# Performance work log

Hardware: AMD Instinct MI355X
Metric: run time of the kernel (lower is better)

Reference implementation:

```python
import jax, jax.numpy as jnp
import numpy as np

EPS = 1e-12  # guard sqrt at zero distance


def setup_inputs() -> dict:
    key = jax.random.key(0)
    k1, k2 = jax.random.split(key)
    B, C, N = 4, 3, 8192
    predict_pc = jax.random.normal(k1, (B, C, N), dtype=jnp.float32)
    gt_pc = jax.random.normal(k2, (B, C, N), dtype=jnp.float32)
    return {"predict_pc": predict_pc, "gt_pc": gt_pc}


def reference(predict_pc, gt_pc):
    # predict_pc: [B, 3, Np], gt_pc: [B, 3, Ng]
    B = gt_pc.shape[0]
    Np = predict_pc.shape[2]
    Ng = gt_pc.shape[2]
    denom = B * (Ng + Np)

    # Pairwise Euclidean distances d[b, n, m] = ||predict[b,:,n] - gt[b,:,m]||
    # via the |p|^2 + |g|^2 - 2 p.g expansion (avoids [B,3,Np,Ng] intermediate).
    p2 = jnp.sum(predict_pc * predict_pc, axis=1)            # [B, Np]
    g2 = jnp.sum(gt_pc * gt_pc, axis=1)                      # [B, Ng]
    dot = jnp.einsum('bcn,bcm->bnm', predict_pc, gt_pc)      # [B, Np, Ng]
    d2 = p2[:, :, None] + g2[:, None, :] - 2.0 * dot         # [B, Np, Ng]
    d = jnp.sqrt(jnp.maximum(d2, EPS))

    # z: for each gt point, distance to nearest predicted point -> min over Np
    z = jnp.min(d, axis=1)   # [B, Ng]
    # z_2: for each predicted point, distance to nearest gt point -> min over Ng
    z2 = jnp.min(d, axis=2)  # [B, Np]

    loss = z.sum() / denom + z2.sum() / denom
    return loss
```

## Files before the change

kernel.cpp:

```cpp
#include <hip/hip_runtime.h>
#include <math.h>


#define B_        4
#define N_        8192
#define THREADS   256
#define ROWS_PB   256
#define ROWBLKS   (N_ / ROWS_PB)
#define MRANGE    1024
#define MSPLIT    (N_ / MRANGE)
#define MTILES    (MRANGE / 16)
#define NGROUPS   B_
#define BLKS_PER_GROUP (ROWBLKS * MSPLIT)
#define POISON    0xAAAAAAAAu
#define INF_BITS  0x7F800000u

typedef __bf16 bf16x8 __attribute__((ext_vector_type(8)));
typedef float  f32x4  __attribute__((ext_vector_type(4)));

#define SM_ZERO   0
#define SM_A      16
#define SM_B      8208
#define SM_COL    40976
#define SM_ROW    45072
#define SM_BYTES  46096

__device__ __forceinline__ unsigned short bf16_rne(float f) {
    unsigned u = __float_as_uint(f);
    return (unsigned short)((u + 0x7FFFu + ((u >> 16) & 1u)) >> 16);
}
__device__ __forceinline__ float bf16_tof(unsigned short h) {
    return __uint_as_float(((unsigned)h) << 16);
}

__device__ __forceinline__ void slotsA(const float* base, int n, unsigned short* dst) {
    float x = base[n], y = base[N_ + n], z = base[2 * N_ + n];
    float p2 = fmaf(x, x, fmaf(y, y, z * z));
    unsigned short hx = bf16_rne(x), hy = bf16_rne(y), hz = bf16_rne(z);
    float lxf = x - bf16_tof(hx), lyf = y - bf16_tof(hy), lzf = z - bf16_tof(hz);
    unsigned short mhx = bf16_rne(-2.0f * bf16_tof(hx));
    unsigned short mhy = bf16_rne(-2.0f * bf16_tof(hy));
    unsigned short mhz = bf16_rne(-2.0f * bf16_tof(hz));
    unsigned short mlx = bf16_rne(-2.0f * bf16_tof(bf16_rne(lxf)));
    unsigned short mly = bf16_rne(-2.0f * bf16_tof(bf16_rne(lyf)));
    unsigned short mlz = bf16_rne(-2.0f * bf16_tof(bf16_rne(lzf)));
    unsigned short p2h = bf16_rne(p2);
    unsigned short p2l = bf16_rne(p2 - bf16_tof(p2h));
    const unsigned short ONE = 0x3F80;
    dst[0] = mhx;  dst[1] = mhy;  dst[2] = mhz;
    dst[3] = mhx;  dst[4] = mhy;  dst[5] = mhz;
    dst[6] = mlx;  dst[7] = mly;  dst[8] = mlz;
    dst[9] = p2h;  dst[10] = p2l; dst[11] = ONE; dst[12] = ONE;
    dst[13] = mlx; dst[14] = mly; dst[15] = mlz;
}

__device__ __forceinline__ void slotsB(const float* base, int m, unsigned short* dst) {
    float x = base[m], y = base[N_ + m], z = base[2 * N_ + m];
    float g2 = fmaf(x, x, fmaf(y, y, z * z));
    unsigned short hx = bf16_rne(x), hy = bf16_rne(y), hz = bf16_rne(z);
    unsigned short lx = bf16_rne(x - bf16_tof(hx));
    unsigned short ly = bf16_rne(y - bf16_tof(hy));
    unsigned short lz = bf16_rne(z - bf16_tof(hz));
    unsigned short g2h = bf16_rne(g2);
    unsigned short g2l = bf16_rne(g2 - bf16_tof(g2h));
    const unsigned short ONE = 0x3F80;
    dst[0] = hx;  dst[1] = hy;  dst[2] = hz;
    dst[3] = lx;  dst[4] = ly;  dst[5] = lz;
    dst[6] = hx;  dst[7] = hy;  dst[8] = hz;
    dst[9] = ONE; dst[10] = ONE; dst[11] = g2h; dst[12] = g2l;
    dst[13] = lx; dst[14] = ly; dst[15] = lz;
}


__global__ __launch_bounds__(THREADS, 3)
void chamfer_mfma_kernel(const float* __restrict__ P, const float* __restrict__ G,
                         unsigned* __restrict__ mins, unsigned* __restrict__ gcnt,
                         unsigned* __restrict__ fcnt, float* __restrict__ gsum,
                         float* __restrict__ out)
{
    __shared__ __align__(16) char smem[SM_BYTES];
    __shared__ float red[THREADS];
    __shared__ unsigned s_ticket;

    const int t      = threadIdx.x;
    const int rowblk = blockIdx.x;
    const int mspl   = blockIdx.y;
    const int b      = blockIdx.z;
    const int rowbase = rowblk * ROWS_PB;
    const int mbase   = mspl * MRANGE;

    const float* Pb = P + (size_t)b * 3 * N_;
    const float* Gb = G + (size_t)b * 3 * N_;

    if (t < 4) ((unsigned*)(smem + SM_ZERO))[t] = 0u;
    unsigned* colmin = (unsigned*)(smem + SM_COL);
    unsigned* rowmin = (unsigned*)(smem + SM_ROW);
#pragma unroll
    for (int k = 0; k < 4; ++k) colmin[k * THREADS + t] = INF_BITS;
    rowmin[t] = INF_BITS;

    slotsA(Pb, rowbase + t, (unsigned short*)(smem + SM_A) + t * 16);
#pragma unroll
    for (int k = 0; k < 4; ++k)
        slotsB(Gb, mbase + k * THREADS + t,
               (unsigned short*)(smem + SM_B) + (k * THREADS + t) * 16);
    __syncthreads();

    const int wave = t >> 6, lane = t & 63, quad = lane >> 4, col = lane & 15;

    bf16x8 afrag[4];
#pragma unroll
    for (int rt = 0; rt < 4; ++rt) {
        const int rowl = wave * 64 + rt * 16 + col;
        const char* ap = (quad < 2) ? (smem + SM_A + rowl * 32 + quad * 16)
                                    : (smem + SM_ZERO);
        afrag[rt] = *(const bf16x8*)ap;
    }
    const char* bp = (quad < 2) ? (smem + SM_B + col * 32 + quad * 16)
                                : (smem + SM_ZERO);
    const int binc = (quad < 2) ? 16 * 32 : 0;

    float rmin[4][4];
#pragma unroll
    for (int rt = 0; rt < 4; ++rt)
#pragma unroll
        for (int r = 0; r < 4; ++r) rmin[rt][r] = 3.4e38f;

    for (int mt = 0; mt < MTILES; ++mt) {
        bf16x8 bfrag = *(const bf16x8*)bp;
        bp += binc;
        float cp = 3.4e38f;
#pragma unroll
        for (int rt = 0; rt < 4; ++rt) {
            f32x4 z = {0.0f, 0.0f, 0.0f, 0.0f};
            f32x4 acc = __builtin_amdgcn_mfma_f32_16x16x32_bf16(afrag[rt], bfrag, z, 0, 0, 0);
            rmin[rt][0] = fminf(rmin[rt][0], acc[0]);
            rmin[rt][1] = fminf(rmin[rt][1], acc[1]);
            rmin[rt][2] = fminf(rmin[rt][2], acc[2]);
            rmin[rt][3] = fminf(rmin[rt][3], acc[3]);
            cp = fminf(cp, fminf(fminf(acc[0], acc[1]), fminf(acc[2], acc[3])));
        }
        atomicMin(&colmin[mt * 16 + col], __float_as_uint(fmaxf(cp, 1e-12f)));
    }

#pragma unroll
    for (int rt = 0; rt < 4; ++rt)
#pragma unroll
        for (int r = 0; r < 4; ++r)
            atomicMin(&rowmin[wave * 64 + rt * 16 + quad * 4 + r],
                      __float_as_uint(fmaxf(rmin[rt][r], 1e-12f)));
    __syncthreads();

    atomicMin(&mins[(size_t)b * N_ + rowbase + t], rowmin[t]);
#pragma unroll
    for (int k = 0; k < 4; ++k) {
        const int i = k * THREADS + t;
        atomicMin(&mins[32768 + (size_t)b * N_ + mbase + i], colmin[i]);
    }

    __syncthreads();
    if (t == 0) {
        __threadfence();
        s_ticket = atomicAdd(&gcnt[b], 1u);
    }
    __syncthreads();
    if (s_ticket != POISON + (unsigned)(BLKS_PER_GROUP - 1)) return;

    __threadfence();
    const uint4* v0 = (const uint4*)(mins + (size_t)b * N_);
    const uint4* v1 = (const uint4*)(mins + 32768 + (size_t)b * N_);
    float acc = 0.0f;
#pragma unroll
    for (int k = 0; k < N_ / 4 / THREADS; ++k) {
        uint4 q = v0[k * THREADS + t];
        uint4 w = v1[k * THREADS + t];
        acc += sqrtf(__uint_as_float(q.x)) + sqrtf(__uint_as_float(q.y))
             + sqrtf(__uint_as_float(q.z)) + sqrtf(__uint_as_float(q.w))
             + sqrtf(__uint_as_float(w.x)) + sqrtf(__uint_as_float(w.y))
             + sqrtf(__uint_as_float(w.z)) + sqrtf(__uint_as_float(w.w));
    }
    red[t] = acc;
    __syncthreads();
    for (int off = 128; off > 0; off >>= 1) {
        if (t < off) red[t] += red[t + off];
        __syncthreads();
    }
    if (t == 0) {
        gsum[b] = red[0];
        __threadfence();
        s_ticket = atomicAdd(fcnt, 1u);
    }
    __syncthreads();
    if (s_ticket != POISON + (unsigned)(NGROUPS - 1)) return;

    __threadfence();
    if (t == 0)
        out[0] = (gsum[0] + gsum[1] + gsum[2] + gsum[3]) * (1.0f / 65536.0f);
}

extern "C" void kernel_launch(void* const* d_in, const int* in_sizes, int n_in,
                              void* d_out, int out_size, void* d_ws, size_t ws_size,
                              hipStream_t stream)
{
    const float* P = (const float*)d_in[0];
    const float* G = (const float*)d_in[1];
    float* out = (float*)d_out;

    unsigned* w    = (unsigned*)d_ws;
    unsigned* mins = w;
    unsigned* gcnt = w + 65536;
    unsigned* fcnt = w + 65600;
    float*    gsum = (float*)(w + 65664);

    dim3 grid(ROWBLKS, MSPLIT, B_);
    chamfer_mfma_kernel<<<grid, THREADS, 0, stream>>>(P, G, mins, gcnt, fcnt, gsum, out);
}
```

Measured before the change: 112.6 us.

## Switch to 32x32x16 MFMA with split K-halves and per-wave column minima

```diff
diff --git a/kernel.cpp b/kernel.cpp
--- a/kernel.cpp
+++ b/kernel.cpp
@@ -7,23 +7,21 @@
 #define THREADS   256
 #define ROWS_PB   256
 #define ROWBLKS   (N_ / ROWS_PB)
-#define MRANGE    1024
+#define MRANGE    512
 #define MSPLIT    (N_ / MRANGE)
-#define MTILES    (MRANGE / 16)
-#define NGROUPS   B_
+#define MTILES    (MRANGE / 32)
 #define BLKS_PER_GROUP (ROWBLKS * MSPLIT)
 #define POISON    0xAAAAAAAAu
 #define INF_BITS  0x7F800000u
 
 typedef __bf16 bf16x8 __attribute__((ext_vector_type(8)));
-typedef float  f32x4  __attribute__((ext_vector_type(4)));
-
-#define SM_ZERO   0
-#define SM_A      16
-#define SM_B      8208
-#define SM_COL    40976
-#define SM_ROW    45072
-#define SM_BYTES  46096
+typedef float  f32x16 __attribute__((ext_vector_type(16)));
+
+#define SM_A      0
+#define SM_B      8192
+#define SM_COL    24576
+#define SM_ROW    32768
+#define SM_BYTES  33792
 
 __device__ __forceinline__ unsigned short bf16_rne(float f) {
     unsigned u = __float_as_uint(f);
@@ -71,8 +69,19 @@
     dst[13] = lx; dst[14] = ly; dst[15] = lz;
 }
 
-
-__global__ __launch_bounds__(THREADS, 3)
+__device__ __forceinline__ float min16(const f32x16& a) {
+    float c0 = fminf(fminf(a[0],  a[1]),  a[2]);
+    float c1 = fminf(fminf(a[3],  a[4]),  a[5]);
+    float c2 = fminf(fminf(a[6],  a[7]),  a[8]);
+    float c3 = fminf(fminf(a[9],  a[10]), a[11]);
+    float c4 = fminf(fminf(a[12], a[13]), a[14]);
+    float c5 = fminf(fminf(c0, c1), a[15]);
+    float c6 = fminf(fminf(c2, c3), c4);
+    return fminf(c5, c6);
+}
+
+
+__global__ __launch_bounds__(THREADS, 4)
 void chamfer_mfma_kernel(const float* __restrict__ P, const float* __restrict__ G,
                          unsigned* __restrict__ mins, unsigned* __restrict__ gcnt,
                          unsigned* __restrict__ fcnt, float* __restrict__ gsum,
@@ -92,70 +101,74 @@
     const float* Pb = P + (size_t)b * 3 * N_;
     const float* Gb = G + (size_t)b * 3 * N_;
 
-    if (t < 4) ((unsigned*)(smem + SM_ZERO))[t] = 0u;
-    unsigned* colmin = (unsigned*)(smem + SM_COL);
     unsigned* rowmin = (unsigned*)(smem + SM_ROW);
-#pragma unroll
-    for (int k = 0; k < 4; ++k) colmin[k * THREADS + t] = INF_BITS;
+    float*    colw   = (float*)(smem + SM_COL);
+
+    {
+        unsigned short s[16];
+        slotsA(Pb, rowbase + t, s);
+        *(ulonglong2*)(smem + SM_A + t * 16)        = *(ulonglong2*)&s[0];
+        *(ulonglong2*)(smem + SM_A + 4096 + t * 16) = *(ulonglong2*)&s[8];
+#pragma unroll
+        for (int k = 0; k < 2; ++k) {
+            const int m = k * THREADS + t;
+            slotsB(Gb, mbase + m, s);
+            *(ulonglong2*)(smem + SM_B + m * 16)        = *(ulonglong2*)&s[0];
+            *(ulonglong2*)(smem + SM_B + 8192 + m * 16) = *(ulonglong2*)&s[8];
+        }
+    }
     rowmin[t] = INF_BITS;
-
-    slotsA(Pb, rowbase + t, (unsigned short*)(smem + SM_A) + t * 16);
-#pragma unroll
-    for (int k = 0; k < 4; ++k)
-        slotsB(Gb, mbase + k * THREADS + t,
-               (unsigned short*)(smem + SM_B) + (k * THREADS + t) * 16);
-    __syncthreads();
-
-    const int wave = t >> 6, lane = t & 63, quad = lane >> 4, col = lane & 15;
-
-    bf16x8 afrag[4];
-#pragma unroll
-    for (int rt = 0; rt < 4; ++rt) {
-        const int rowl = wave * 64 + rt * 16 + col;
-        const char* ap = (quad < 2) ? (smem + SM_A + rowl * 32 + quad * 16)
-                                    : (smem + SM_ZERO);
-        afrag[rt] = *(const bf16x8*)ap;
-    }
-    const char* bp = (quad < 2) ? (smem + SM_B + col * 32 + quad * 16)
-                                : (smem + SM_ZERO);
-    const int binc = (quad < 2) ? 16 * 32 : 0;
-
-    float rmin[4][4];
-#pragma unroll
-    for (int rt = 0; rt < 4; ++rt)
-#pragma unroll
-        for (int r = 0; r < 4; ++r) rmin[rt][r] = 3.4e38f;
+    __syncthreads();
+
+    const int lane = t & 63, wave = t >> 6;
+    const int half = lane >> 5;
+    const int lrow = lane & 31;
+
+    bf16x8 afrag[2];
+#pragma unroll
+    for (int rt = 0; rt < 2; ++rt)
+        afrag[rt] = *(const bf16x8*)(smem + SM_A + half * 4096
+                                     + (wave * 64 + rt * 32 + lrow) * 16);
+
+    const char* bbase = smem + SM_B + half * 8192 + lrow * 16;
+
+    f32x16 zero16 = {0.0f,0.0f,0.0f,0.0f,0.0f,0.0f,0.0f,0.0f,
+                     0.0f,0.0f,0.0f,0.0f,0.0f,0.0f,0.0f,0.0f};
+    float rmin0[16], rmin1[16];
+#pragma unroll
+    for (int r = 0; r < 16; ++r) { rmin0[r] = 3.4e38f; rmin1[r] = 3.4e38f; }
 
     for (int mt = 0; mt < MTILES; ++mt) {
-        bf16x8 bfrag = *(const bf16x8*)bp;
-        bp += binc;
-        float cp = 3.4e38f;
-#pragma unroll
-        for (int rt = 0; rt < 4; ++rt) {
-            f32x4 z = {0.0f, 0.0f, 0.0f, 0.0f};
-            f32x4 acc = __builtin_amdgcn_mfma_f32_16x16x32_bf16(afrag[rt], bfrag, z, 0, 0, 0);
-            rmin[rt][0] = fminf(rmin[rt][0], acc[0]);
-            rmin[rt][1] = fminf(rmin[rt][1], acc[1]);
-            rmin[rt][2] = fminf(rmin[rt][2], acc[2]);
-            rmin[rt][3] = fminf(rmin[rt][3], acc[3]);
-            cp = fminf(cp, fminf(fminf(acc[0], acc[1]), fminf(acc[2], acc[3])));
+        bf16x8 bfrag = *(const bf16x8*)(bbase + mt * 32 * 16);
+        f32x16 acc0 = __builtin_amdgcn_mfma_f32_32x32x16_bf16(afrag[0], bfrag, zero16, 0, 0, 0);
+        f32x16 acc1 = __builtin_amdgcn_mfma_f32_32x32x16_bf16(afrag[1], bfrag, zero16, 0, 0, 0);
+#pragma unroll
+        for (int r = 0; r < 16; ++r) {
+            rmin0[r] = fminf(rmin0[r], acc0[r]);
+            rmin1[r] = fminf(rmin1[r], acc1[r]);
         }
-        atomicMin(&colmin[mt * 16 + col], __float_as_uint(fmaxf(cp, 1e-12f)));
-    }
-
-#pragma unroll
-    for (int rt = 0; rt < 4; ++rt)
-#pragma unroll
-        for (int r = 0; r < 4; ++r)
-            atomicMin(&rowmin[wave * 64 + rt * 16 + quad * 4 + r],
-                      __float_as_uint(fmaxf(rmin[rt][r], 1e-12f)));
+        float cp = fminf(min16(acc0), min16(acc1));
+        cp = fminf(cp, __shfl_xor(cp, 32, 64));
+        if (lane < 32) colw[wave * MRANGE + mt * 32 + lrow] = cp;
+    }
+
+#pragma unroll
+    for (int r = 0; r < 16; ++r) {
+        const int row0 = wave * 64 +      (r & 3) + 8 * (r >> 2) + 4 * half;
+        const int row1 = wave * 64 + 32 + (r & 3) + 8 * (r >> 2) + 4 * half;
+        atomicMin(&rowmin[row0], __float_as_uint(fmaxf(rmin0[r], 1e-12f)));
+        atomicMin(&rowmin[row1], __float_as_uint(fmaxf(rmin1[r], 1e-12f)));
+    }
     __syncthreads();
 
     atomicMin(&mins[(size_t)b * N_ + rowbase + t], rowmin[t]);
 #pragma unroll
-    for (int k = 0; k < 4; ++k) {
-        const int i = k * THREADS + t;
-        atomicMin(&mins[32768 + (size_t)b * N_ + mbase + i], colmin[i]);
+    for (int k = 0; k < 2; ++k) {
+        const int m = k * THREADS + t;
+        float cm = fminf(fminf(colw[m], colw[MRANGE + m]),
+                         fminf(colw[2 * MRANGE + m], colw[3 * MRANGE + m]));
+        atomicMin(&mins[32768 + (size_t)b * N_ + mbase + m],
+                  __float_as_uint(fmaxf(cm, 1e-12f)));
     }
 
     __syncthreads();
@@ -191,7 +204,7 @@
         s_ticket = atomicAdd(fcnt, 1u);
     }
     __syncthreads();
-    if (s_ticket != POISON + (unsigned)(NGROUPS - 1)) return;
+    if (s_ticket != POISON + (unsigned)(B_ - 1)) return;
 
     __threadfence();
     if (t == 0)
```

Result: slower. 146.6 us (+30.2%).
